# Kernel tuning notes

Measured on AMD Instinct MI355X. Metric: run time of the kernel, lower is better.

## Reference

```python
import jax, jax.numpy as jnp
import numpy as np

N_LIT, N_CLAUSE, N_EDGES, D = 100000, 400000, 1200000, 128


def setup_inputs() -> dict:
    key = jax.random.key(0)
    ks = jax.random.split(key, 9)
    s = 1.0 / np.sqrt(D)  # PyTorch LSTM init: U(-1/sqrt(hidden), 1/sqrt(hidden))
    x_l = jax.random.normal(ks[0], (N_LIT, D), jnp.float32)
    h0 = jax.random.normal(ks[1], (N_CLAUSE, D), jnp.float32)
    c0 = jax.random.normal(ks[2], (N_CLAUSE, D), jnp.float32)
    W_ih = jax.random.uniform(ks[3], (4 * D, D), jnp.float32, -s, s)
    W_hh = jax.random.uniform(ks[4], (4 * D, D), jnp.float32, -s, s)
    b_ih = jax.random.uniform(ks[5], (4 * D,), jnp.float32, -s, s)
    b_hh = jax.random.uniform(ks[6], (4 * D,), jnp.float32, -s, s)
    edge_lit = jax.random.randint(ks[7], (N_EDGES,), 0, N_LIT, jnp.int32)
    edge_clause = jnp.sort(jax.random.randint(ks[8], (N_EDGES,), 0, N_CLAUSE, jnp.int32))
    return {"x_l": x_l, "h0": h0, "c0": c0, "W_ih": W_ih, "W_hh": W_hh,
            "b_ih": b_ih, "b_hh": b_hh, "edge_lit": edge_lit, "edge_clause": edge_clause}


def reference(x_l, h0, c0, W_ih, W_hh, b_ih, b_hh, edge_lit, edge_clause):
    n_clauses = h0.shape[0]
    # msg = adj_t @ x_l : sparse aggregation of literal features into clauses
    msg = jax.ops.segment_sum(x_l[edge_lit], edge_clause, num_segments=n_clauses)  # [n_clauses, D]
    # Single-timestep LSTM cell (seq_len=1, batch=n_clauses); PyTorch gate order i,f,g,o
    gates = msg @ W_ih.T + b_ih + h0 @ W_hh.T + b_hh  # [n_clauses, 4D]
    i, f, g, o = jnp.split(gates, 4, axis=-1)
    i = jax.nn.sigmoid(i)
    f = jax.nn.sigmoid(f)
    g = jnp.tanh(g)
    o = jax.nn.sigmoid(o)
    c_new = f * c0 + i * g
    h_new = o * jnp.tanh(c_new)
    return (h_new, c_new)
```

## Files before the change

kernel.cpp:

```cpp
#include <hip/hip_runtime.h>
#include <hip/hip_bf16.h>


using frag_ab = __attribute__((ext_vector_type(8))) short;
using frag_cd = __attribute__((ext_vector_type(4))) float;

__device__ __forceinline__ float bf2f(unsigned short u) {
    union { unsigned u; float f; } v; v.u = ((unsigned)u) << 16; return v.f;
}
__device__ __forceinline__ unsigned short f2bf(float f) {
    __hip_bfloat16 h = __float2bfloat16(f);
    return *reinterpret_cast<unsigned short*>(&h);
}
__device__ __forceinline__ float sigm(float x) {
    return __builtin_amdgcn_rcpf(1.0f + __builtin_amdgcn_exp2f(-1.442695040889f * x));
}
__device__ __forceinline__ float tanh_fast(float x) {
    float s = __builtin_amdgcn_rcpf(1.0f + __builtin_amdgcn_exp2f(-2.885390081777f * x));
    return __builtin_fmaf(2.0f, s, -1.0f);
}
__device__ __forceinline__ frag_ab load8_fp32(const float* p) {
    float4 a = *reinterpret_cast<const float4*>(p);
    float4 b = *reinterpret_cast<const float4*>(p + 4);
    frag_ab r;
    r[0] = (short)f2bf(a.x); r[1] = (short)f2bf(a.y);
    r[2] = (short)f2bf(a.z); r[3] = (short)f2bf(a.w);
    r[4] = (short)f2bf(b.x); r[5] = (short)f2bf(b.y);
    r[6] = (short)f2bf(b.z); r[7] = (short)f2bf(b.w);
    return r;
}

#define WS_BPACK_OFF  0
#define WS_BIAS_OFF   262144
#define WS_FLAG_OFF   264192
#define WS_ROWPTR_OFF 264704

#define EDGE_CAP 512

__global__ void detect_fmt(const unsigned short* __restrict__ x, int* __restrict__ flag) {
    int t = threadIdx.x;
    int cnt = 0;
    for (int i = t; i < 4096; i += 64) {
        unsigned e = (x[2 * i] >> 7) & 0xFF;
        cnt += (e >= 0xC0) ? 1 : 0;
    }
    #pragma unroll
    for (int s = 32; s; s >>= 1) cnt += __shfl_xor(cnt, s);
    if (t == 0) *flag = (cnt > 64) ? 1 : 0;
}

__global__ void build_rowptr(const int* __restrict__ edge_clause, int* __restrict__ rowptr,
                             int n_edges, int n_clause) {
    int idx = blockIdx.x * blockDim.x + threadIdx.x;
    if (idx > n_clause) return;
    int lo = 0, hi = n_edges;
    while (lo < hi) {
        int mid = (lo + hi) >> 1;
        if (edge_clause[mid] < idx) lo = mid + 1; else hi = mid;
    }
    rowptr[idx] = lo;
}

template <int FP32IN>
__global__ void prepack(const void* __restrict__ W_ih_, const void* __restrict__ W_hh_,
                        const void* __restrict__ b_ih_, const void* __restrict__ b_hh_,
                        unsigned short* __restrict__ Bpack, float* __restrict__ bias,
                        const int* __restrict__ flag) {
    if (*flag != FP32IN) return;
    int idx = blockIdx.x * blockDim.x + threadIdx.x;
    if (idx < 16384) {
        int kk = idx >> 11;
        int n  = (idx >> 2) & 511;
        int lq = idx & 3;
        int ksrc = (kk & 3) * 32 + lq * 8;
        frag_ab v;
        if constexpr (FP32IN) {
            const float* W = (kk < 4) ? (const float*)W_ih_ : (const float*)W_hh_;
            v = load8_fp32(W + (size_t)n * 128 + ksrc);
        } else {
            const unsigned short* W =
                (kk < 4) ? (const unsigned short*)W_ih_ : (const unsigned short*)W_hh_;
            v = *reinterpret_cast<const frag_ab*>(W + (size_t)n * 128 + ksrc);
        }
        *reinterpret_cast<frag_ab*>(Bpack + (size_t)idx * 8) = v;
    }
    if (idx < 512) {
        float b;
        if constexpr (FP32IN)
            b = ((const float*)b_ih_)[idx] + ((const float*)b_hh_)[idx];
        else
            b = bf2f(((const unsigned short*)b_ih_)[idx]) +
                bf2f(((const unsigned short*)b_hh_)[idx]);
        bias[idx] = b;
    }
}

__global__ void prepack_xl(const float* __restrict__ x_l,
                           unsigned short* __restrict__ xlb,
                           const int* __restrict__ flag, int n_chunks) {
    if (*flag != 1) return;
    int idx = blockIdx.x * blockDim.x + threadIdx.x;
    if (idx >= n_chunks) return;
    frag_ab v = load8_fp32(x_l + (size_t)idx * 8);
    *reinterpret_cast<frag_ab*>(xlb + (size_t)idx * 8) = v;
}

template <int FP32IN>
__global__ __launch_bounds__(512, 8) void gather_msg(
    const void* __restrict__ x_l_,
    const void* __restrict__ xlb_,
    const int*  __restrict__ rowptr_g,
    const int*  __restrict__ edge_lit,
    void* __restrict__ out_,
    const int* __restrict__ fmt_flag,
    int n_clause)
{
    if (*fmt_flag != FP32IN) return;

    __shared__ int elits[EDGE_CAP];
    const int tid  = threadIdx.x;
    const int lane = tid & 63;
    const int w    = tid >> 6;
    const int cbase = blockIdx.x * 64;

    const unsigned short* xl = FP32IN ? (const unsigned short*)xlb_
                                      : (const unsigned short*)x_l_;

    unsigned short* msgb;
    if constexpr (FP32IN) msgb = (unsigned short*)((float*)out_ + (size_t)n_clause * 128);
    else                  msgb = (unsigned short*)out_ + (size_t)n_clause * 128;
    constexpr int MSTRIDE = FP32IN ? 256 : 128;

    int rp_l = 0;
    if (lane < 9) rp_l = rowptr_g[cbase + w * 8 + lane];
    const int eBase = rowptr_g[cbase];
    const int eEnd  = rowptr_g[cbase + 64];
    const int eCount = eEnd - eBase;
    for (int i = tid; i < eCount && i < EDGE_CAP; i += 512)
        elits[i] = edge_lit[eBase + i];
    __syncthreads();

    const int q   = lane >> 4;
    const int l16 = lane & 15;
    for (int s = 0; s < 8; ++s) {
        int st = __shfl(rp_l, s)     - eBase;
        int en = __shfl(rp_l, s + 1) - eBase;
        float a[8] = {0.f, 0.f, 0.f, 0.f, 0.f, 0.f, 0.f, 0.f};
        for (int e = st + q; e < en; e += 4) {
            int lit = (e < EDGE_CAP) ? elits[e] : edge_lit[eBase + e];
            frag_ab v = *reinterpret_cast<const frag_ab*>(
                xl + (size_t)lit * 128 + l16 * 8);
            #pragma unroll
            for (int j = 0; j < 8; ++j) a[j] += bf2f((unsigned short)v[j]);
        }
        #pragma unroll
        for (int j = 0; j < 8; ++j) {
            a[j] += __shfl_xor(a[j], 16);
            a[j] += __shfl_xor(a[j], 32);
        }
        if (q == 0) {
            frag_ab o;
            #pragma unroll
            for (int j = 0; j < 8; ++j) o[j] = (short)f2bf(a[j]);
            *reinterpret_cast<frag_ab*>(
                msgb + (size_t)(cbase + w * 8 + s) * MSTRIDE + l16 * 8) = o;
        }
    }
}

template <int FP32IN>
__global__ __launch_bounds__(512, 4) void gemm_lstm(
    const void* __restrict__ h0_,
    const void* __restrict__ c0_,
    const unsigned short* __restrict__ Bpack,
    const float* __restrict__ bias,
    void* __restrict__ out_,
    const int* __restrict__ fmt_flag,
    int n_clause)
{
    if (*fmt_flag != FP32IN) return;

    __shared__ __align__(16) unsigned char SH[32768];
    unsigned char* Amsg = SH;
    unsigned char* Ah0  = SH + 16384;
    float* LDSf = (float*)SH;

    const int tid  = threadIdx.x;
    const int lane = tid & 63;
    const int w    = tid >> 6;
    const int cbase = blockIdx.x * 64;

    unsigned short* msgb;
    if constexpr (FP32IN) msgb = (unsigned short*)((float*)out_ + (size_t)n_clause * 128);
    else                  msgb = (unsigned short*)out_ + (size_t)n_clause * 128;
    constexpr int MSTRIDE = FP32IN ? 256 : 128;

    #pragma unroll
    for (int q0 = 0; q0 < 2; ++q0) {
        int q = tid + q0 * 512;
        int row = q >> 4;
        int j   = q & 15;
        frag_ab v = *reinterpret_cast<const frag_ab*>(
            msgb + (size_t)(cbase + row) * MSTRIDE + j * 8);
        int byte = (j * 16) ^ ((row & 7) << 4);
        *reinterpret_cast<frag_ab*>(Amsg + row * 256 + byte) = v;
    }
    #pragma unroll
    for (int q0 = 0; q0 < 2; ++q0) {
        int q = tid + q0 * 512;
        int row = q >> 4;
        int j   = q & 15;
        frag_ab v;
        if constexpr (FP32IN) {
            v = load8_fp32((const float*)h0_ + (size_t)(cbase + row) * 128 + j * 8);
        } else {
            v = *reinterpret_cast<const frag_ab*>(
                (const unsigned short*)h0_ + (size_t)(cbase + row) * 128 + j * 8);
        }
        int byte = (j * 16) ^ ((row & 7) << 4);
        *reinterpret_cast<frag_ab*>(Ah0 + row * 256 + byte) = v;
    }
    __syncthreads();

    const int l15 = lane & 15;
    const int lq  = lane >> 4;
    const int d = w * 16 + l15;

    float cold[4][4];
    #pragma unroll
    for (int mf = 0; mf < 4; ++mf) {
        #pragma unroll
        for (int r = 0; r < 4; ++r) {
            int m = cbase + mf * 16 + lq * 4 + r;
            if constexpr (FP32IN) cold[mf][r] = ((const float*)c0_)[(size_t)m * 128 + d];
            else cold[mf][r] = bf2f(((const unsigned short*)c0_)[(size_t)m * 128 + d]);
        }
    }

    frag_cd acc[4][4];
    #pragma unroll
    for (int g = 0; g < 4; ++g)
        #pragma unroll
        for (int mf = 0; mf < 4; ++mf)
            acc[g][mf] = (frag_cd){0.f, 0.f, 0.f, 0.f};

    const frag_ab* Bp = reinterpret_cast<const frag_ab*>(Bpack);
    float bi[4];
    #pragma unroll
    for (int g = 0; g < 4; ++g) bi[g] = bias[g * 128 + d];

    #pragma unroll
    for (int kk = 0; kk < 8; ++kk) {
        const unsigned char* At = (kk < 4) ? Amsg : Ah0;
        frag_ab afr[4];
        #pragma unroll
        for (int mf = 0; mf < 4; ++mf) {
            int row = mf * 16 + l15;
            int byte = ((kk & 3) * 64 + lq * 16) ^ ((row & 7) << 4);
            afr[mf] = *reinterpret_cast<const frag_ab*>(At + row * 256 + byte);
        }
        frag_ab bfr[4];
        #pragma unroll
        for (int g = 0; g < 4; ++g) {
            int n = g * 128 + w * 16 + l15;
            bfr[g] = Bp[(kk * 512 + n) * 4 + lq];
        }
        #pragma unroll
        for (int g = 0; g < 4; ++g)
            #pragma unroll
            for (int mf = 0; mf < 4; ++mf)
                acc[g][mf] = __builtin_amdgcn_mfma_f32_16x16x32_bf16(
                    afr[mf], bfr[g], acc[g][mf], 0, 0, 0);
    }

    #pragma unroll
    for (int mf = 0; mf < 4; ++mf) {
        #pragma unroll
        for (int r = 0; r < 4; ++r) {
            float gi = acc[0][mf][r] + bi[0];
            float gf = acc[1][mf][r] + bi[1];
            float gg = acc[2][mf][r] + bi[2];
            float go = acc[3][mf][r] + bi[3];
            float iv = sigm(gi);
            float fv = sigm(gf);
            float gv = tanh_fast(gg);
            float ov = sigm(go);
            float cn = fv * cold[mf][r] + iv * gv;
            float hn = ov * tanh_fast(cn);
            acc[0][mf][r] = hn;
            acc[1][mf][r] = cn;
        }
    }

    #pragma unroll
    for (int half = 0; half < 2; ++half) {
        __syncthreads();
        #pragma unroll
        for (int mf = 0; mf < 4; ++mf) {
            #pragma unroll
            for (int r = 0; r < 4; ++r) {
                int rl = mf * 16 + lq * 4 + r;
                int idx = rl * 128 + ((((d >> 2) ^ (rl & 7)) << 2) | (d & 3));
                LDSf[idx] = acc[half][mf][r];
            }
        }
        __syncthreads();
        if constexpr (FP32IN) {
            float* outp = (float*)out_ + (size_t)half * n_clause * 128;
            #pragma unroll
            for (int q0 = 0; q0 < 4; ++q0) {
                int q = tid + q0 * 512;
                int row = q >> 5;
                int j   = q & 31;
                float4 v = *reinterpret_cast<const float4*>(
                    &LDSf[row * 128 + ((j ^ (row & 7)) << 2)]);
                *reinterpret_cast<float4*>(outp + (size_t)(cbase + row) * 128 + j * 4) = v;
            }
        } else {
            unsigned short* outp = (unsigned short*)out_ + (size_t)half * n_clause * 128;
            #pragma unroll
            for (int q0 = 0; q0 < 2; ++q0) {
                int q = tid + q0 * 512;
                int row = q >> 4;
                int jj  = q & 15;
                int j0 = 2 * jj, j1 = 2 * jj + 1;
                float4 f0 = *reinterpret_cast<const float4*>(
                    &LDSf[row * 128 + ((j0 ^ (row & 7)) << 2)]);
                float4 f1 = *reinterpret_cast<const float4*>(
                    &LDSf[row * 128 + ((j1 ^ (row & 7)) << 2)]);
                frag_ab o;
                o[0] = (short)f2bf(f0.x); o[1] = (short)f2bf(f0.y);
                o[2] = (short)f2bf(f0.z); o[3] = (short)f2bf(f0.w);
                o[4] = (short)f2bf(f1.x); o[5] = (short)f2bf(f1.y);
                o[6] = (short)f2bf(f1.z); o[7] = (short)f2bf(f1.w);
                *reinterpret_cast<frag_ab*>(outp + (size_t)(cbase + row) * 128 + jj * 8) = o;
            }
        }
    }
}

extern "C" void kernel_launch(void* const* d_in, const int* in_sizes, int n_in,
                              void* d_out, int out_size, void* d_ws, size_t ws_size,
                              hipStream_t stream) {
    const void* x_l  = d_in[0];
    const void* h0   = d_in[1];
    const void* c0   = d_in[2];
    const void* W_ih = d_in[3];
    const void* W_hh = d_in[4];
    const void* b_ih = d_in[5];
    const void* b_hh = d_in[6];
    const int* edge_lit    = (const int*)d_in[7];
    const int* edge_clause = (const int*)d_in[8];

    int n_edges  = in_sizes[7];
    int n_lit    = in_sizes[0] / 128;
    int n_clause = in_sizes[1] / 128;
    int nblocks  = (n_clause + 63) / 64;

    unsigned char* ws = (unsigned char*)d_ws;
    unsigned short* Bpack = (unsigned short*)(ws + WS_BPACK_OFF);
    float* bias  = (float*)(ws + WS_BIAS_OFF);
    int* flag    = (int*)(ws + WS_FLAG_OFF);
    int* rowptr  = (int*)(ws + WS_ROWPTR_OFF);

    unsigned short* xlb = (unsigned short*)d_out;

    detect_fmt<<<1, 64, 0, stream>>>((const unsigned short*)x_l, flag);

    build_rowptr<<<(n_clause + 256) / 256, 256, 0, stream>>>(
        edge_clause, rowptr, n_edges, n_clause);

    prepack<1><<<64, 256, 0, stream>>>(W_ih, W_hh, b_ih, b_hh, Bpack, bias, flag);
    prepack<0><<<64, 256, 0, stream>>>(W_ih, W_hh, b_ih, b_hh, Bpack, bias, flag);

    int n_chunks = n_lit * 16;
    prepack_xl<<<(n_chunks + 255) / 256, 256, 0, stream>>>(
        (const float*)x_l, xlb, flag, n_chunks);

    gather_msg<1><<<nblocks, 512, 0, stream>>>(
        x_l, xlb, rowptr, edge_lit, d_out, flag, n_clause);
    gather_msg<0><<<nblocks, 512, 0, stream>>>(
        x_l, xlb, rowptr, edge_lit, d_out, flag, n_clause);

    gemm_lstm<1><<<nblocks, 512, 0, stream>>>(
        h0, c0, Bpack, bias, d_out, flag, n_clause);
    gemm_lstm<0><<<nblocks, 512, 0, stream>>>(
        h0, c0, Bpack, bias, d_out, flag, n_clause);
}
```

Baseline: 373.3 us.

## Write pre-swizzled LDS image in gather and async-copy it into GEMM LDS

The gather kernel now writes the message tile, and for fp32 inputs also the bf16-converted h0 tile, into a per-block pre-swizzled image laid out exactly like the GEMM's shared-memory tiles. The GEMM kernel then fills shared memory with direct global-to-LDS 16-byte loads instead of loading into registers, swizzling and storing. The barrier is moved after the c0 loads so those overlap the async copies. This removes the register round trip and the h0 conversion from the GEMM stage, at the cost of a larger scratch image in the output buffer and more work in the gather kernel.

Result: slower. 579.7 us (+55.3%).

```diff
diff --git a/kernel.cpp b/kernel.cpp
--- a/kernel.cpp
+++ b/kernel.cpp
@@ -28,6 +28,11 @@
     r[4] = (short)f2bf(b.x); r[5] = (short)f2bf(b.y);
     r[6] = (short)f2bf(b.z); r[7] = (short)f2bf(b.w);
     return r;
+}
+__device__ __forceinline__ void gload16(const void* g, void* l) {
+    __builtin_amdgcn_global_load_lds(
+        (const __attribute__((address_space(1))) unsigned int*)g,
+        (__attribute__((address_space(3))) unsigned int*)l, 16, 0, 0);
 }
 
 #define WS_BPACK_OFF  0
@@ -106,9 +111,10 @@
 }
 
 template <int FP32IN>
-__global__ __launch_bounds__(512, 8) void gather_msg(
+__global__ __launch_bounds__(512, 8) void gather_image(
     const void* __restrict__ x_l_,
     const void* __restrict__ xlb_,
+    const void* __restrict__ h0_,
     const int*  __restrict__ rowptr_g,
     const int*  __restrict__ edge_lit,
     void* __restrict__ out_,
@@ -125,11 +131,11 @@
 
     const unsigned short* xl = FP32IN ? (const unsigned short*)xlb_
                                       : (const unsigned short*)x_l_;
-
-    unsigned short* msgb;
-    if constexpr (FP32IN) msgb = (unsigned short*)((float*)out_ + (size_t)n_clause * 128);
-    else                  msgb = (unsigned short*)out_ + (size_t)n_clause * 128;
-    constexpr int MSTRIDE = FP32IN ? 256 : 128;
+    unsigned char* img;
+    if constexpr (FP32IN)
+        img = (unsigned char*)out_ + (size_t)n_clause * 512 + (size_t)blockIdx.x * 32768;
+    else
+        img = (unsigned char*)out_ + (size_t)n_clause * 256 + (size_t)blockIdx.x * 16384;
 
     int rp_l = 0;
     if (lane < 9) rp_l = rowptr_g[cbase + w * 8 + lane];
@@ -138,6 +144,18 @@
     const int eCount = eEnd - eBase;
     for (int i = tid; i < eCount && i < EDGE_CAP; i += 512)
         elits[i] = edge_lit[eBase + i];
+
+    if constexpr (FP32IN) {
+        #pragma unroll
+        for (int q0 = 0; q0 < 2; ++q0) {
+            int q = tid + q0 * 512;
+            int row = q >> 4;
+            int j   = q & 15;
+            frag_ab v = load8_fp32((const float*)h0_ + (size_t)(cbase + row) * 128 + j * 8);
+            *reinterpret_cast<frag_ab*>(
+                img + 16384 + row * 256 + ((j * 16) ^ ((row & 7) << 4))) = v;
+        }
+    }
     __syncthreads();
 
     const int q   = lane >> 4;
@@ -159,11 +177,12 @@
             a[j] += __shfl_xor(a[j], 32);
         }
         if (q == 0) {
+            int cc = w * 8 + s;
             frag_ab o;
             #pragma unroll
             for (int j = 0; j < 8; ++j) o[j] = (short)f2bf(a[j]);
             *reinterpret_cast<frag_ab*>(
-                msgb + (size_t)(cbase + w * 8 + s) * MSTRIDE + l16 * 8) = o;
+                img + cc * 256 + ((l16 * 16) ^ ((cc & 7) << 4))) = o;
         }
     }
 }
@@ -190,37 +209,34 @@
     const int w    = tid >> 6;
     const int cbase = blockIdx.x * 64;
 
-    unsigned short* msgb;
-    if constexpr (FP32IN) msgb = (unsigned short*)((float*)out_ + (size_t)n_clause * 128);
-    else                  msgb = (unsigned short*)out_ + (size_t)n_clause * 128;
-    constexpr int MSTRIDE = FP32IN ? 256 : 128;
-
-    #pragma unroll
-    for (int q0 = 0; q0 < 2; ++q0) {
-        int q = tid + q0 * 512;
-        int row = q >> 4;
-        int j   = q & 15;
-        frag_ab v = *reinterpret_cast<const frag_ab*>(
-            msgb + (size_t)(cbase + row) * MSTRIDE + j * 8);
-        int byte = (j * 16) ^ ((row & 7) << 4);
-        *reinterpret_cast<frag_ab*>(Amsg + row * 256 + byte) = v;
-    }
-    #pragma unroll
-    for (int q0 = 0; q0 < 2; ++q0) {
-        int q = tid + q0 * 512;
-        int row = q >> 4;
-        int j   = q & 15;
-        frag_ab v;
-        if constexpr (FP32IN) {
-            v = load8_fp32((const float*)h0_ + (size_t)(cbase + row) * 128 + j * 8);
-        } else {
-            v = *reinterpret_cast<const frag_ab*>(
-                (const unsigned short*)h0_ + (size_t)(cbase + row) * 128 + j * 8);
-        }
-        int byte = (j * 16) ^ ((row & 7) << 4);
-        *reinterpret_cast<frag_ab*>(Ah0 + row * 256 + byte) = v;
-    }
-    __syncthreads();
+    const unsigned char* img;
+    if constexpr (FP32IN)
+        img = (const unsigned char*)out_ + (size_t)n_clause * 512 + (size_t)blockIdx.x * 32768;
+    else
+        img = (const unsigned char*)out_ + (size_t)n_clause * 256 + (size_t)blockIdx.x * 16384;
+
+    if constexpr (FP32IN) {
+        #pragma unroll
+        for (int q0 = 0; q0 < 4; ++q0) {
+            int off = q0 * 8192 + w * 1024;
+            gload16(img + off + lane * 16, SH + off);
+        }
+    } else {
+        #pragma unroll
+        for (int q0 = 0; q0 < 2; ++q0) {
+            int off = q0 * 8192 + w * 1024;
+            gload16(img + off + lane * 16, Amsg + off);
+        }
+        const unsigned short* h0s = (const unsigned short*)h0_;
+        #pragma unroll
+        for (int q0 = 0; q0 < 2; ++q0) {
+            int chunk = q0 * 512 + w * 64 + lane;
+            int row = chunk >> 4, j = chunk & 15;
+            const unsigned short* src =
+                h0s + (size_t)(cbase + row) * 128 + (j ^ (row & 7)) * 8;
+            gload16(src, Ah0 + (q0 * 512 + w * 64) * 16);
+        }
+    }
 
     const int l15 = lane & 15;
     const int lq  = lane >> 4;
@@ -236,6 +252,7 @@
             else cold[mf][r] = bf2f(((const unsigned short*)c0_)[(size_t)m * 128 + d]);
         }
     }
+    __syncthreads();
 
     frag_cd acc[4][4];
     #pragma unroll
@@ -309,9 +326,9 @@
             float* outp = (float*)out_ + (size_t)half * n_clause * 128;
             #pragma unroll
             for (int q0 = 0; q0 < 4; ++q0) {
-                int q = tid + q0 * 512;
-                int row = q >> 5;
-                int j   = q & 31;
+                int qq = tid + q0 * 512;
+                int row = qq >> 5;
+                int j   = qq & 31;
                 float4 v = *reinterpret_cast<const float4*>(
                     &LDSf[row * 128 + ((j ^ (row & 7)) << 2)]);
                 *reinterpret_cast<float4*>(outp + (size_t)(cbase + row) * 128 + j * 4) = v;
@@ -320,9 +337,9 @@
             unsigned short* outp = (unsigned short*)out_ + (size_t)half * n_clause * 128;
             #pragma unroll
             for (int q0 = 0; q0 < 2; ++q0) {
-                int q = tid + q0 * 512;
-                int row = q >> 4;
-                int jj  = q & 15;
+                int qq = tid + q0 * 512;
+                int row = qq >> 4;
+                int jj  = qq & 15;
                 int j0 = 2 * jj, j1 = 2 * jj + 1;
                 float4 f0 = *reinterpret_cast<const float4*>(
                     &LDSf[row * 128 + ((j0 ^ (row & 7)) << 2)]);
@@ -377,10 +394,10 @@
     prepack_xl<<<(n_chunks + 255) / 256, 256, 0, stream>>>(
         (const float*)x_l, xlb, flag, n_chunks);
 
-    gather_msg<1><<<nblocks, 512, 0, stream>>>(
-        x_l, xlb, rowptr, edge_lit, d_out, flag, n_clause);
-    gather_msg<0><<<nblocks, 512, 0, stream>>>(
-        x_l, xlb, rowptr, edge_lit, d_out, flag, n_clause);
+    gather_image<1><<<nblocks, 512, 0, stream>>>(
+        x_l, xlb, h0, rowptr, edge_lit, d_out, flag, n_clause);
+    gather_image<0><<<nblocks, 512, 0, stream>>>(
+        x_l, xlb, h0, rowptr, edge_lit, d_out, flag, n_clause);
 
     gemm_lstm<1><<<nblocks, 512, 0, stream>>>(
         h0, c0, Bpack, bias, d_out, flag, n_clause);
```
